# Optimization experiments

Hardware: AMD Instinct MI355X
Metric: run time of the kernel (lower is better)

The kernel has to match this reference:

```python
import jax, jax.numpy as jnp
import numpy as np

N_EMBD = 1024
N_HEAD = 16
HEAD_DIM = N_EMBD // N_HEAD


def setup_inputs() -> dict:
    key = jax.random.key(0)
    kx, kqkv, kw, kb = jax.random.split(key, 4)
    B, T = 4, 2048
    x = jax.random.normal(kx, (B, T, N_EMBD), dtype=jnp.float32)
    # nn.Linear weights stored [out, in]; apply as x @ W.T
    w_qkv = jax.random.normal(kqkv, (3 * N_EMBD, N_EMBD), dtype=jnp.float32) * (N_EMBD ** -0.5)
    w_out = jax.random.normal(kw, (N_EMBD, N_EMBD), dtype=jnp.float32) * (N_EMBD ** -0.5)
    b_out = jax.random.normal(kb, (N_EMBD,), dtype=jnp.float32) * 0.01
    return {"x": x, "w_qkv": w_qkv, "w_out": w_out, "b_out": b_out}


def reference(x, w_qkv, w_out, b_out):
    B, T, C = x.shape
    H, D = N_HEAD, HEAD_DIM
    qkv = jnp.einsum('btc,fc->btf', x, w_qkv)  # [B,T,3C]
    q, k, v = jnp.split(qkv, 3, axis=-1)
    q = q.reshape(B, T, H, D).transpose(0, 2, 1, 3)  # [B,H,T,D]
    k = k.reshape(B, T, H, D).transpose(0, 2, 1, 3)
    v = v.reshape(B, T, H, D).transpose(0, 2, 1, 3)
    att = jnp.einsum('bhqd,bhkd->bhqk', q, k) * (D ** -0.5)  # [B,H,T,T]
    causal = jnp.tril(jnp.ones((T, T), dtype=bool))
    att = jnp.where(causal[None, None], att, jnp.float32(-jnp.inf))
    att = jax.nn.softmax(att, axis=-1)
    out = jnp.einsum('bhqk,bhkd->bhqd', att, v)  # [B,H,T,D]
    out = out.transpose(0, 2, 1, 3).reshape(B, T, C)
    return jnp.einsum('btc,oc->bto', out, w_out) + b_out
```

## Files before the change

### kernel.cpp

```cpp
#include <hip/hip_runtime.h>
#include <stdint.h>

#define SEQ 2048
#define C3 3072
#define C1 1024

typedef __bf16 bf16x8 __attribute__((ext_vector_type(8)));
typedef short short8 __attribute__((ext_vector_type(8)));
typedef float f32x4 __attribute__((ext_vector_type(4)));
typedef float f32x16 __attribute__((ext_vector_type(16)));
typedef const __attribute__((address_space(1))) void gv_t;
typedef __attribute__((address_space(3))) void lv_t;

#if __has_builtin(__builtin_amdgcn_exp2f)
#define EXP2(x) __builtin_amdgcn_exp2f(x)
#else
#define EXP2(x) exp2f(x)
#endif

static __device__ __forceinline__ unsigned short f2bf(float f) {
  union { float ff; unsigned u; } x; x.ff = f;
  unsigned u = x.u + 0x7FFFu + ((x.u >> 16) & 1u);
  return (unsigned short)(u >> 16);
}
static __device__ __forceinline__ unsigned rne2(float lo, float hi) {
  return (unsigned)f2bf(lo) | ((unsigned)f2bf(hi) << 16);
}
static __device__ __forceinline__ unsigned pk2(float lo, float hi) {
  union { float f; unsigned u; } a, b; a.f = lo; b.f = hi;
  return __builtin_amdgcn_perm(b.u, a.u, 0x07060302);
}

__global__ void k_cvt3(const float* __restrict__ ia, const float* __restrict__ ib,
                       const float* __restrict__ ic, unsigned short* __restrict__ oa,
                       unsigned short* __restrict__ ob, unsigned short* __restrict__ oc) {
  int blk = blockIdx.x;
  const float* in; unsigned short* out; int base;
  if (blk < 8192)      { in = ia; out = oa; base = blk; }
  else if (blk < 11264){ in = ib; out = ob; base = blk - 8192; }
  else                 { in = ic; out = oc; base = blk - 11264; }
  int i = base * 256 + threadIdx.x;
  f32x4 v = ((const f32x4*)in)[i];
  ushort4 o;
  o.x = f2bf(v[0]); o.y = f2bf(v[1]); o.z = f2bf(v[2]); o.w = f2bf(v[3]);
  ((ushort4*)out)[i] = o;
}

template<int MODE>
__global__ __launch_bounds__(256, 3) void k_gemm(
    const unsigned short* __restrict__ A, const unsigned short* __restrict__ B,
    void* __restrict__ Cout, const float* __restrict__ bias,
    unsigned short* __restrict__ vTout, int M, int N, int K)
{
  __shared__ unsigned short As[128 * 64];
  __shared__ unsigned short Bs[128 * 64];
  const int tid = threadIdx.x;
  const int w = tid >> 6, l = tid & 63;
  const int lane15 = l & 15, quad = l >> 4;
  const int m0 = blockIdx.y * 128, n0 = blockIdx.x * 128;
  const int wm = (w >> 1) * 64, wn = (w & 1) * 64;

  f32x4 acc[4][4];
#pragma unroll
  for (int i = 0; i < 4; i++)
#pragma unroll
    for (int j = 0; j < 4; j++) acc[i][j] = (f32x4){0.f, 0.f, 0.f, 0.f};

  const int srow = l >> 3;
  const int g_off = ((l & 7) ^ (srow & 7)) * 8;
  const unsigned short* Ab = A + (size_t)(m0 + w * 32 + srow) * K + g_off;
  const unsigned short* Bb = B + (size_t)(n0 + w * 32 + srow) * K + g_off;
  const int rsl = lane15 & 7;

  for (int k0 = 0; k0 < K; k0 += 64) {
    __syncthreads();
#pragma unroll
    for (int i = 0; i < 4; i++) {
      int rb = w * 32 + i * 8;
      __builtin_amdgcn_global_load_lds((gv_t*)(Ab + (size_t)(i * 8) * K + k0),
                                       (lv_t*)&As[rb * 64], 16, 0, 0);
      __builtin_amdgcn_global_load_lds((gv_t*)(Bb + (size_t)(i * 8) * K + k0),
                                       (lv_t*)&Bs[rb * 64], 16, 0, 0);
    }
    __syncthreads();
#pragma unroll
    for (int s = 0; s < 2; s++) {
      bf16x8 af[4], bfr[4];
      const int slot = ((s * 4 + quad) ^ rsl) * 8;
#pragma unroll
      for (int t = 0; t < 4; t++) {
        af[t]  = *(const bf16x8*)&As[(wm + t * 16 + lane15) * 64 + slot];
        bfr[t] = *(const bf16x8*)&Bs[(wn + t * 16 + lane15) * 64 + slot];
      }
#pragma unroll
      for (int i = 0; i < 4; i++)
#pragma unroll
        for (int j = 0; j < 4; j++)
          acc[i][j] = __builtin_amdgcn_mfma_f32_16x16x32_bf16(af[i], bfr[j], acc[i][j], 0, 0, 0);
    }
  }

  if (MODE == 0) {
    if (n0 >= 2048) {
#pragma unroll
      for (int i = 0; i < 4; i++) {
        int rowb = m0 + wm + i * 16 + quad * 4;
        int bb = rowb >> 11, t = rowb & 2047;
#pragma unroll
        for (int j = 0; j < 4; j++) {
          int hd = n0 + wn + j * 16 + lane15 - 2048;
          unsigned short* vp = vTout +
              ((size_t)((bb << 4) + (hd >> 6)) * 64 + (hd & 63)) * SEQ + t;
          *(uint2*)vp = make_uint2(rne2(acc[i][j][0], acc[i][j][1]),
                                   rne2(acc[i][j][2], acc[i][j][3]));
        }
      }
    } else {
      unsigned short* Cp = (unsigned short*)Cout;
      const float s = (n0 < 1024) ? 0.18033688f : 1.0f;
#pragma unroll
      for (int i = 0; i < 4; i++) {
        int rowb = m0 + wm + i * 16 + quad * 4;
#pragma unroll
        for (int j = 0; j < 4; j++) {
          int col = n0 + wn + j * 16 + lane15;
#pragma unroll
          for (int r = 0; r < 4; r++)
            Cp[(size_t)(rowb + r) * N + col] = f2bf(acc[i][j][r] * s);
        }
      }
    }
  } else {
    float* Cp = (float*)Cout;
#pragma unroll
    for (int i = 0; i < 4; i++) {
      int rowb = m0 + wm + i * 16 + quad * 4;
#pragma unroll
      for (int j = 0; j < 4; j++) {
        int col = n0 + wn + j * 16 + lane15;
        float bv = bias[col];
#pragma unroll
        for (int r = 0; r < 4; r++)
          Cp[(size_t)(rowb + r) * N + col] = acc[i][j][r] + bv;
      }
    }
  }
}


static __device__ __forceinline__ void stage_kv(
    unsigned short* bufp, const unsigned short* __restrict__ qkv,
    const unsigned short* __restrict__ vT, size_t tokb, int bh, int h,
    int k0, int w, int krow_l, int kslot, int vrow_l, int vslot)
{
  unsigned short* Kb = bufp;
  unsigned short* Vb = bufp + 8192;
#pragma unroll
  for (int i = 0; i < 4; i++) {
    int rb = (w * 4 + i) * 8;
    int row = rb + krow_l;
    int ck = kslot ^ (row & 7);
    const unsigned short* g = qkv + (tokb + k0 + row) * C3 + C1 + h * 64 + ck * 8;
    __builtin_amdgcn_global_load_lds((gv_t*)g, (lv_t*)&Kb[rb * 64], 16, 0, 0);
  }
#pragma unroll
  for (int i = 0; i < 4; i++) {
    int rb = (w * 4 + i) * 4;
    int row = rb + vrow_l;
    int ck = vslot ^ (row & 15);
    const unsigned short* g = vT + ((size_t)bh * 64 + row) * SEQ + k0 + ck * 8;
    __builtin_amdgcn_global_load_lds((gv_t*)g, (lv_t*)&Vb[rb * 128], 16, 0, 0);
  }
}

static __device__ __forceinline__ void attn_tile(
    f32x16* O, float& lrun, const bf16x8* qf,
    const unsigned short* Kb, const unsigned short* Vb,
    bool diag, int k0, int qmy, int w, int l31, int hl)
{
#pragma unroll
  for (int ht = 0; ht < 2; ht++) {
    if (diag && (ht * 2 > w)) continue;
    const bool two = !diag || (ht * 2 + 1 <= w);

#pragma unroll
    for (int lm = 0; lm < 2; lm++) {
      if (lm == 1 && !two) continue;
      const int mt = ht * 2 + lm;

      f32x16 stL;
#pragma unroll
      for (int i = 0; i < 16; i++) stL[i] = 0.f;
      {
        int row = mt * 32 + l31;
        const unsigned short* kr = &Kb[row * 64];
        __builtin_amdgcn_s_setprio(1);
#pragma unroll
        for (int ks = 0; ks < 4; ks++) {
          bf16x8 a = *(const bf16x8*)&kr[((((ks << 1) | hl)) ^ (row & 7)) * 8];
          stL = __builtin_amdgcn_mfma_f32_32x32x16_bf16(a, qf[ks], stL, 0, 0, 0);
        }
        __builtin_amdgcn_s_setprio(0);
      }

      if (diag && mt == w) {
#pragma unroll
        for (int r = 0; r < 16; r++) {
          int key = k0 + w * 32 + (r & 3) + ((r >> 2) << 3) + (hl << 2);
          if (key > qmy) stL[r] = -1e30f;
        }
      }

      float ps0 = 0.f, ps1 = 0.f, ps2 = 0.f, ps3 = 0.f;
      unsigned pk[8];
#pragma unroll
      for (int r = 0; r < 16; r += 4) {
        float p0 = EXP2(stL[r]     - 16.f);
        float p1 = EXP2(stL[r + 1] - 16.f);
        float p2 = EXP2(stL[r + 2] - 16.f);
        float p3 = EXP2(stL[r + 3] - 16.f);
        ps0 += p0; ps1 += p1; ps2 += p2; ps3 += p3;
        pk[(r >> 1)]     = pk2(p0, p1);
        pk[(r >> 1) + 1] = pk2(p2, p3);
      }
      lrun += (ps0 + ps1) + (ps2 + ps3);

#pragma unroll
      for (int e = 0; e < 2; e++) {
        unsigned pA0 = pk[4 * e], pA1 = pk[4 * e + 1];
        unsigned pB0 = pk[4 * e + 2], pB1 = pk[4 * e + 3];
        unsigned w0 = hl ? pA0 : pB0, w1 = hl ? pA1 : pB1;
        unsigned r0 = (unsigned)__shfl_xor((int)w0, 32, 64);
        unsigned r1 = (unsigned)__shfl_xor((int)w1, 32, 64);
        unsigned s0 = hl ? pB0 : pA0, s1 = hl ? pB1 : pA1;
        union { unsigned u[4]; bf16x8 v; } Bf;
        Bf.u[0] = hl ? r0 : s0; Bf.u[1] = hl ? r1 : s1;
        Bf.u[2] = hl ? s0 : r0; Bf.u[3] = hl ? s1 : r1;
        int kk = ht * 4 + lm * 2 + e;
        __builtin_amdgcn_s_setprio(1);
#pragma unroll
        for (int dt = 0; dt < 2; dt++) {
          int row = dt * 32 + l31;
          bf16x8 a = *(const bf16x8*)&Vb[row * 128 + (((2 * kk + hl)) ^ (row & 15)) * 8];
          O[dt] = __builtin_amdgcn_mfma_f32_32x32x16_bf16(a, Bf.v, O[dt], 0, 0, 0);
        }
        __builtin_amdgcn_s_setprio(0);
      }
    }
  }
}

static __device__ __forceinline__ void attn_epi(
    const f32x16* O, float lrun, unsigned short* buf,
    unsigned short* __restrict__ att, size_t tokb, int q0, int h,
    int w, int l, int l31, int hl)
{
  lrun += __shfl_xor(lrun, 32, 64);
  float linv = __builtin_amdgcn_rcpf(lrun);
  unsigned* epi32 = (unsigned*)buf;
  const int base = w * 2304 + l31 * 72;
  __builtin_amdgcn_s_waitcnt(0);
#pragma unroll
  for (int dt = 0; dt < 2; dt++)
#pragma unroll
    for (int c = 0; c < 4; c++) {
      int d0 = dt * 32 + c * 8 + hl * 4;
      epi32[(base + d0) >> 1]     = rne2(O[dt][4 * c] * linv, O[dt][4 * c + 1] * linv);
      epi32[(base + d0 + 2) >> 1] = rne2(O[dt][4 * c + 2] * linv, O[dt][4 * c + 3] * linv);
    }
  __builtin_amdgcn_s_waitcnt(0);
  {
    int q = l >> 1, hf = l & 1;
    const unsigned short* ep = &buf[w * 2304 + q * 72 + hf * 32];
    unsigned short* og = att + (tokb + q0 + w * 32 + q) * C1 + h * 64 + hf * 32;
#pragma unroll
    for (int c2 = 0; c2 < 4; c2++)
      *(bf16x8*)(og + c2 * 8) = *(const bf16x8*)&ep[c2 * 8];
  }
}

__global__ __launch_bounds__(256, 2) void k_attn(
    const unsigned short* __restrict__ qkv, const unsigned short* __restrict__ vT,
    unsigned short* __restrict__ att)
{
  __shared__ unsigned short buf[2][16384];
  const int tid = threadIdx.x;
  const int w = tid >> 6, l = tid & 63;
  const int l31 = l & 31, hl = l >> 5;
  const int bh = blockIdx.x, b = bh >> 4, h = bh & 15;
  const int yq = blockIdx.y;
  const int qt_lo = yq, qt_hi = 15 - yq;
  const int q0l = qt_lo << 7, q0h = qt_hi << 7;
  const int nkt = qt_hi + 1;
  const size_t tokb = (size_t)b * SEQ;
  const int qmy_l = q0l + w * 32 + l31;
  const int qmy_h = q0h + w * 32 + l31;

  const int krow_l = l >> 3, kslot = l & 7;
  const int vrow_l = l >> 4, vslot = l & 15;

  bf16x8 qfh[4], qfl[4];
  {
    const unsigned short* qph = qkv + (tokb + q0h + w * 32 + l31) * C3 + h * 64 + hl * 8;
    const unsigned short* qpl = qkv + (tokb + q0l + w * 32 + l31) * C3 + h * 64 + hl * 8;
#pragma unroll
    for (int ks = 0; ks < 4; ks++) {
      qfh[ks] = *(const bf16x8*)(qph + ks * 16);
      qfl[ks] = *(const bf16x8*)(qpl + ks * 16);
    }
  }

  f32x16 Oh[2], Ol[2];
#pragma unroll
  for (int i = 0; i < 16; i++) { Oh[0][i] = 0.f; Oh[1][i] = 0.f; Ol[0][i] = 0.f; Ol[1][i] = 0.f; }
  float lrh = 0.f, lrl = 0.f;

  stage_kv(&buf[0][0], qkv, vT, tokb, bh, h, 0, w, krow_l, kslot, vrow_l, vslot);

  int cur = 0;
  for (int kt = 0; kt < nkt; kt++) {
    asm volatile("s_waitcnt vmcnt(0)" ::: "memory");
    __builtin_amdgcn_s_barrier();
    if (kt + 1 < nkt)
      stage_kv(&buf[cur ^ 1][0], qkv, vT, tokb, bh, h, (kt + 1) << 7,
               w, krow_l, kslot, vrow_l, vslot);

    const unsigned short* Kb = &buf[cur][0];
    const unsigned short* Vb = &buf[cur][8192];
    const int k0 = kt << 7;

    attn_tile(Oh, lrh, qfh, Kb, Vb, kt == qt_hi, k0, qmy_h, w, l31, hl);
    if (kt <= qt_lo)
      attn_tile(Ol, lrl, qfl, Kb, Vb, kt == qt_lo, k0, qmy_l, w, l31, hl);

    cur ^= 1;
  }

  __syncthreads();
  attn_epi(Oh, lrh, &buf[0][0], att, tokb, q0h, h, w, l, l31, hl);
  attn_epi(Ol, lrl, &buf[0][0], att, tokb, q0l, h, w, l, l31, hl);
}

extern "C" void kernel_launch(void* const* d_in, const int* in_sizes, int n_in,
                              void* d_out, int out_size, void* d_ws, size_t ws_size,
                              hipStream_t stream) {
  const float* x     = (const float*)d_in[0];
  const float* w_qkv = (const float*)d_in[1];
  const float* w_out = (const float*)d_in[2];
  const float* b_out = (const float*)d_in[3];
  float* out = (float*)d_out;

  unsigned short* xb  = (unsigned short*)d_ws;
  unsigned short* wqb = xb  + (size_t)8192 * 1024;
  unsigned short* wob = wqb + (size_t)3072 * 1024;
  unsigned short* qkv = wob + (size_t)1024 * 1024;
  unsigned short* att = qkv + (size_t)8192 * 3072;
  unsigned short* vT  = att + (size_t)8192 * 1024;

  k_cvt3<<<12288, 256, 0, stream>>>(x, w_qkv, w_out, xb, wqb, wob);
  k_gemm<0><<<dim3(24, 64), 256, 0, stream>>>(xb, wqb, (void*)qkv, nullptr, vT, 8192, 3072, 1024);
  k_attn<<<dim3(64, 8), 256, 0, stream>>>(qkv, vT, att);
  k_gemm<1><<<dim3(8, 64), 256, 0, stream>>>(att, wob, (void*)out, b_out, nullptr, 8192, 1024, 1024);
}
```

Baseline: 234.5 us.

## Halve attention KV tile to 64 keys to cut LDS and raise occupancy

Shrinks the staged K/V tile in the causal attention kernel from 128 to 64 keys, halving shared memory, and raises launch bounds to allow three blocks per CU. Causal skipping now works per 32-key subtile against each wave's query block rather than per 128-key tile. This is meant to improve latency hiding and trim masked work, at the cost of twice as many barrier and wait rounds and smaller loads per round.

```diff
diff --git a/kernel.cpp b/kernel.cpp
--- a/kernel.cpp
+++ b/kernel.cpp
@@ -151,101 +151,96 @@
 static __device__ __forceinline__ void stage_kv(
     unsigned short* bufp, const unsigned short* __restrict__ qkv,
     const unsigned short* __restrict__ vT, size_t tokb, int bh, int h,
-    int k0, int w, int krow_l, int kslot, int vrow_l, int vslot)
+    int k0, int w, int l)
 {
   unsigned short* Kb = bufp;
-  unsigned short* Vb = bufp + 8192;
-#pragma unroll
-  for (int i = 0; i < 4; i++) {
-    int rb = (w * 4 + i) * 8;
-    int row = rb + krow_l;
-    int ck = kslot ^ (row & 7);
+  unsigned short* Vb = bufp + 4096;
+  const int rl = l >> 3, sl = l & 7;
+#pragma unroll
+  for (int i = 0; i < 2; i++) {
+    int rb = (w * 2 + i) * 8;
+    int row = rb + rl;
+    int ck = sl ^ (row & 7);
     const unsigned short* g = qkv + (tokb + k0 + row) * C3 + C1 + h * 64 + ck * 8;
     __builtin_amdgcn_global_load_lds((gv_t*)g, (lv_t*)&Kb[rb * 64], 16, 0, 0);
   }
 #pragma unroll
-  for (int i = 0; i < 4; i++) {
-    int rb = (w * 4 + i) * 4;
-    int row = rb + vrow_l;
-    int ck = vslot ^ (row & 15);
+  for (int i = 0; i < 2; i++) {
+    int rb = (w * 2 + i) * 8;
+    int row = rb + rl;
+    int ck = sl ^ (row & 7);
     const unsigned short* g = vT + ((size_t)bh * 64 + row) * SEQ + k0 + ck * 8;
-    __builtin_amdgcn_global_load_lds((gv_t*)g, (lv_t*)&Vb[rb * 128], 16, 0, 0);
+    __builtin_amdgcn_global_load_lds((gv_t*)g, (lv_t*)&Vb[rb * 64], 16, 0, 0);
   }
 }
 
 static __device__ __forceinline__ void attn_tile(
     f32x16* O, float& lrun, const bf16x8* qf,
     const unsigned short* Kb, const unsigned short* Vb,
-    bool diag, int k0, int qmy, int w, int l31, int hl)
-{
-#pragma unroll
-  for (int ht = 0; ht < 2; ht++) {
-    if (diag && (ht * 2 > w)) continue;
-    const bool two = !diag || (ht * 2 + 1 <= w);
-
-#pragma unroll
-    for (int lm = 0; lm < 2; lm++) {
-      if (lm == 1 && !two) continue;
-      const int mt = ht * 2 + lm;
-
-      f32x16 stL;
-#pragma unroll
-      for (int i = 0; i < 16; i++) stL[i] = 0.f;
-      {
-        int row = mt * 32 + l31;
-        const unsigned short* kr = &Kb[row * 64];
-        __builtin_amdgcn_s_setprio(1);
-#pragma unroll
-        for (int ks = 0; ks < 4; ks++) {
-          bf16x8 a = *(const bf16x8*)&kr[((((ks << 1) | hl)) ^ (row & 7)) * 8];
-          stL = __builtin_amdgcn_mfma_f32_32x32x16_bf16(a, qf[ks], stL, 0, 0, 0);
-        }
-        __builtin_amdgcn_s_setprio(0);
-      }
-
-      if (diag && mt == w) {
-#pragma unroll
-        for (int r = 0; r < 16; r++) {
-          int key = k0 + w * 32 + (r & 3) + ((r >> 2) << 3) + (hl << 2);
-          if (key > qmy) stL[r] = -1e30f;
-        }
-      }
-
-      float ps0 = 0.f, ps1 = 0.f, ps2 = 0.f, ps3 = 0.f;
-      unsigned pk[8];
-#pragma unroll
-      for (int r = 0; r < 16; r += 4) {
-        float p0 = EXP2(stL[r]     - 16.f);
-        float p1 = EXP2(stL[r + 1] - 16.f);
-        float p2 = EXP2(stL[r + 2] - 16.f);
-        float p3 = EXP2(stL[r + 3] - 16.f);
-        ps0 += p0; ps1 += p1; ps2 += p2; ps3 += p3;
-        pk[(r >> 1)]     = pk2(p0, p1);
-        pk[(r >> 1) + 1] = pk2(p2, p3);
-      }
-      lrun += (ps0 + ps1) + (ps2 + ps3);
-
-#pragma unroll
-      for (int e = 0; e < 2; e++) {
-        unsigned pA0 = pk[4 * e], pA1 = pk[4 * e + 1];
-        unsigned pB0 = pk[4 * e + 2], pB1 = pk[4 * e + 3];
-        unsigned w0 = hl ? pA0 : pB0, w1 = hl ? pA1 : pB1;
-        unsigned r0 = (unsigned)__shfl_xor((int)w0, 32, 64);
-        unsigned r1 = (unsigned)__shfl_xor((int)w1, 32, 64);
-        unsigned s0 = hl ? pB0 : pA0, s1 = hl ? pB1 : pA1;
-        union { unsigned u[4]; bf16x8 v; } Bf;
-        Bf.u[0] = hl ? r0 : s0; Bf.u[1] = hl ? r1 : s1;
-        Bf.u[2] = hl ? s0 : r0; Bf.u[3] = hl ? s1 : r1;
-        int kk = ht * 4 + lm * 2 + e;
-        __builtin_amdgcn_s_setprio(1);
-#pragma unroll
-        for (int dt = 0; dt < 2; dt++) {
-          int row = dt * 32 + l31;
-          bf16x8 a = *(const bf16x8*)&Vb[row * 128 + (((2 * kk + hl)) ^ (row & 15)) * 8];
-          O[dt] = __builtin_amdgcn_mfma_f32_32x32x16_bf16(a, Bf.v, O[dt], 0, 0, 0);
-        }
-        __builtin_amdgcn_s_setprio(0);
-      }
+    int kb0, int qw, int qmy, int l31, int hl)
+{
+#pragma unroll
+  for (int lm = 0; lm < 2; lm++) {
+    const int kb = kb0 + lm * 32;
+    if (kb > qw + 31) continue;
+
+    f32x16 stL;
+#pragma unroll
+    for (int i = 0; i < 16; i++) stL[i] = 0.f;
+    {
+      int row = lm * 32 + l31;
+      const unsigned short* kr = &Kb[row * 64];
+      __builtin_amdgcn_s_setprio(1);
+#pragma unroll
+      for (int ks = 0; ks < 4; ks++) {
+        bf16x8 a = *(const bf16x8*)&kr[((((ks << 1) | hl)) ^ (row & 7)) * 8];
+        stL = __builtin_amdgcn_mfma_f32_32x32x16_bf16(a, qf[ks], stL, 0, 0, 0);
+      }
+      __builtin_amdgcn_s_setprio(0);
+    }
+
+    if (kb == qw) {
+#pragma unroll
+      for (int r = 0; r < 16; r++) {
+        int key = kb + (r & 3) + ((r >> 2) << 3) + (hl << 2);
+        if (key > qmy) stL[r] = -1e30f;
+      }
+    }
+
+    float ps0 = 0.f, ps1 = 0.f, ps2 = 0.f, ps3 = 0.f;
+    unsigned pk[8];
+#pragma unroll
+    for (int r = 0; r < 16; r += 4) {
+      float p0 = EXP2(stL[r]     - 16.f);
+      float p1 = EXP2(stL[r + 1] - 16.f);
+      float p2 = EXP2(stL[r + 2] - 16.f);
+      float p3 = EXP2(stL[r + 3] - 16.f);
+      ps0 += p0; ps1 += p1; ps2 += p2; ps3 += p3;
+      pk[(r >> 1)]     = pk2(p0, p1);
+      pk[(r >> 1) + 1] = pk2(p2, p3);
+    }
+    lrun += (ps0 + ps1) + (ps2 + ps3);
+
+#pragma unroll
+    for (int e = 0; e < 2; e++) {
+      unsigned pA0 = pk[4 * e], pA1 = pk[4 * e + 1];
+      unsigned pB0 = pk[4 * e + 2], pB1 = pk[4 * e + 3];
+      unsigned w0 = hl ? pA0 : pB0, w1 = hl ? pA1 : pB1;
+      unsigned r0 = (unsigned)__shfl_xor((int)w0, 32, 64);
+      unsigned r1 = (unsigned)__shfl_xor((int)w1, 32, 64);
+      unsigned s0 = hl ? pB0 : pA0, s1 = hl ? pB1 : pA1;
+      union { unsigned u[4]; bf16x8 v; } Bf;
+      Bf.u[0] = hl ? r0 : s0; Bf.u[1] = hl ? r1 : s1;
+      Bf.u[2] = hl ? s0 : r0; Bf.u[3] = hl ? s1 : r1;
+      int kk = lm * 2 + e;
+      __builtin_amdgcn_s_setprio(1);
+#pragma unroll
+      for (int dt = 0; dt < 2; dt++) {
+        int row = dt * 32 + l31;
+        bf16x8 a = *(const bf16x8*)&Vb[row * 64 + (((2 * kk + hl)) ^ (row & 7)) * 8];
+        O[dt] = __builtin_amdgcn_mfma_f32_32x32x16_bf16(a, Bf.v, O[dt], 0, 0, 0);
+      }
+      __builtin_amdgcn_s_setprio(0);
     }
   }
 }
@@ -279,11 +274,11 @@
   }
 }
 
-__global__ __launch_bounds__(256, 2) void k_attn(
+__global__ __launch_bounds__(256, 3) void k_attn(
     const unsigned short* __restrict__ qkv, const unsigned short* __restrict__ vT,
     unsigned short* __restrict__ att)
 {
-  __shared__ unsigned short buf[2][16384];
+  __shared__ unsigned short buf[2][8192];
   const int tid = threadIdx.x;
   const int w = tid >> 6, l = tid & 63;
   const int l31 = l & 31, hl = l >> 5;
@@ -291,18 +286,16 @@
   const int yq = blockIdx.y;
   const int qt_lo = yq, qt_hi = 15 - yq;
   const int q0l = qt_lo << 7, q0h = qt_hi << 7;
-  const int nkt = qt_hi + 1;
+  const int nr_hi = 2 * qt_hi + 2;
+  const int nr_lo = 2 * qt_lo + 2;
   const size_t tokb = (size_t)b * SEQ;
-  const int qmy_l = q0l + w * 32 + l31;
-  const int qmy_h = q0h + w * 32 + l31;
-
-  const int krow_l = l >> 3, kslot = l & 7;
-  const int vrow_l = l >> 4, vslot = l & 15;
+  const int qw_l = q0l + w * 32, qw_h = q0h + w * 32;
+  const int qmy_l = qw_l + l31, qmy_h = qw_h + l31;
 
   bf16x8 qfh[4], qfl[4];
   {
-    const unsigned short* qph = qkv + (tokb + q0h + w * 32 + l31) * C3 + h * 64 + hl * 8;
-    const unsigned short* qpl = qkv + (tokb + q0l + w * 32 + l31) * C3 + h * 64 + hl * 8;
+    const unsigned short* qph = qkv + (tokb + qw_h + l31) * C3 + h * 64 + hl * 8;
+    const unsigned short* qpl = qkv + (tokb + qw_l + l31) * C3 + h * 64 + hl * 8;
 #pragma unroll
     for (int ks = 0; ks < 4; ks++) {
       qfh[ks] = *(const bf16x8*)(qph + ks * 16);
@@ -315,23 +308,22 @@
   for (int i = 0; i < 16; i++) { Oh[0][i] = 0.f; Oh[1][i] = 0.f; Ol[0][i] = 0.f; Ol[1][i] = 0.f; }
   float lrh = 0.f, lrl = 0.f;
 
-  stage_kv(&buf[0][0], qkv, vT, tokb, bh, h, 0, w, krow_l, kslot, vrow_l, vslot);
+  stage_kv(&buf[0][0], qkv, vT, tokb, bh, h, 0, w, l);
 
   int cur = 0;
-  for (int kt = 0; kt < nkt; kt++) {
+  for (int r = 0; r < nr_hi; r++) {
     asm volatile("s_waitcnt vmcnt(0)" ::: "memory");
     __builtin_amdgcn_s_barrier();
-    if (kt + 1 < nkt)
-      stage_kv(&buf[cur ^ 1][0], qkv, vT, tokb, bh, h, (kt + 1) << 7,
-               w, krow_l, kslot, vrow_l, vslot);
+    if (r + 1 < nr_hi)
+      stage_kv(&buf[cur ^ 1][0], qkv, vT, tokb, bh, h, (r + 1) << 6, w, l);
 
     const unsigned short* Kb = &buf[cur][0];
-    const unsigned short* Vb = &buf[cur][8192];
-    const int k0 = kt << 7;
-
-    attn_tile(Oh, lrh, qfh, Kb, Vb, kt == qt_hi, k0, qmy_h, w, l31, hl);
-    if (kt <= qt_lo)
-      attn_tile(Ol, lrl, qfl, Kb, Vb, kt == qt_lo, k0, qmy_l, w, l31, hl);
+    const unsigned short* Vb = &buf[cur][4096];
+    const int kb0 = r << 6;
+
+    attn_tile(Oh, lrh, qfh, Kb, Vb, kb0, qw_h, qmy_h, l31, hl);
+    if (r < nr_lo)
+      attn_tile(Ol, lrl, qfl, Kb, Vb, kb0, qw_l, qmy_l, l31, hl);
 
     cur ^= 1;
   }
```

New measurement: 244.7 us. +4.3%, slower.
